# Kernel tuning notes

Hardware: AMD Instinct MI355X
Metric: run time of the kernel (lower is better)

The kernel has to match this reference:

```python
import jax, jax.numpy as jnp
import numpy as np

NUM_HEADS = 8
HEAD_DIM = 64
HIDDEN = 512
ROPE_THETA = 500000.0


def _make_rope(seq_len, head_dim, theta):
    inv_freq = 1.0 / (theta ** (np.arange(0, head_dim, 2, dtype=np.float32) / head_dim))
    t = np.arange(seq_len, dtype=np.float32)
    freqs = np.outer(t, inv_freq)                  # [S, hd/2]
    emb = np.concatenate([freqs, freqs], axis=-1)  # [S, hd]
    return jnp.asarray(np.cos(emb)), jnp.asarray(np.sin(emb))


def setup_inputs() -> dict:
    key = jax.random.key(0)
    ks = jax.random.split(key, 5)
    B, S, H = 1, 4096, HIDDEN
    num_registers = 32
    hidden_states = jax.random.normal(ks[0], (B, S, H), dtype=jnp.float32)
    scale = 0.02
    Wq = jax.random.normal(ks[1], (H, H), dtype=jnp.float32) * scale
    Wk = jax.random.normal(ks[2], (H, H), dtype=jnp.float32) * scale
    Wv = jax.random.normal(ks[3], (H, H), dtype=jnp.float32) * scale
    Wo = jax.random.normal(ks[4], (H, H), dtype=jnp.float32) * scale
    cos, sin = _make_rope(S - num_registers, HEAD_DIM, ROPE_THETA)
    return {"hidden_states": hidden_states, "Wq": Wq, "Wk": Wk, "Wv": Wv,
            "Wo": Wo, "cos": cos, "sin": sin, "num_registers": num_registers}


def _rotate_half(x):
    x1, x2 = jnp.split(x, 2, axis=-1)
    return jnp.concatenate([-x2, x1], axis=-1)


def _apply_rope(q, k, cos, sin):
    # cos/sin: [S_real, hd] broadcast over [B, H, S_real, hd]
    cos = cos[None, None]
    sin = sin[None, None]
    return q * cos + _rotate_half(q) * sin, k * cos + _rotate_half(k) * sin


def reference(hidden_states, Wq, Wk, Wv, Wo, cos, sin, num_registers):
    B, S, _ = hidden_states.shape
    def proj(W):
        # torch Linear: x @ W.T -> [B, S, H] -> [B, nh, S, hd]
        y = jnp.einsum('bsh,oh->bso', hidden_states, W)
        return y.reshape(B, S, NUM_HEADS, HEAD_DIM).transpose(0, 2, 1, 3)
    q, k, v = proj(Wq), proj(Wk), proj(Wv)

    if num_registers > 0:
        q_reg, q_real = q[:, :, :num_registers], q[:, :, num_registers:]
        k_reg, k_real = k[:, :, :num_registers], k[:, :, num_registers:]
        q_real, k_real = _apply_rope(q_real, k_real, cos, sin)
        q = jnp.concatenate([q_reg, q_real], axis=2)
        k = jnp.concatenate([k_reg, k_real], axis=2)
    else:
        q, k = _apply_rope(q, k, cos, sin)

    scale = 1.0 / jnp.sqrt(jnp.float32(HEAD_DIM))
    scores = jnp.einsum('bhqd,bhkd->bhqk', q, k) * scale  # [B, nh, S, S]
    causal = jnp.tril(jnp.ones((S, S), dtype=bool))
    scores = jnp.where(causal[None, None], scores, jnp.float32(-1e30))
    attn = jax.nn.softmax(scores, axis=-1)
    out = jnp.einsum('bhqk,bhkd->bhqd', attn, v)
    out = out.transpose(0, 2, 1, 3).reshape(B, S, HIDDEN)
    return jnp.einsum('bsh,oh->bso', out, Wo)
```

## Files before the change

kernel.cpp:

```cpp
#include <hip/hip_runtime.h>
#include <cstdint>
#include <cstddef>

#define S_LEN 4096
#define HID   512
#define NHEAD 8
#define HD    64
#define SCALE_LOG2E 0.1803368801111204f

typedef __bf16 bf16;
typedef __bf16 bf16x8 __attribute__((ext_vector_type(8)));
typedef __bf16 bf16x4 __attribute__((ext_vector_type(4)));
typedef float  f32x4  __attribute__((ext_vector_type(4)));

__global__ __launch_bounds__(256) void cvt_f32_bf16(const float* __restrict__ src,
                                                    bf16* __restrict__ dst, int n) {
    int i = (blockIdx.x * 256 + threadIdx.x) * 4;
    if (i + 3 < n) {
        const float4 v = *(const float4*)(src + i);
        bf16x4 o;
        o[0] = (bf16)v.x; o[1] = (bf16)v.y; o[2] = (bf16)v.z; o[3] = (bf16)v.w;
        *(bf16x4*)(dst + i) = o;
    }
}

__global__ __launch_bounds__(256) void cvt_w4(
    const float* __restrict__ s0, const float* __restrict__ s1,
    const float* __restrict__ s2, const float* __restrict__ s3,
    bf16* __restrict__ d0, bf16* __restrict__ d1,
    bf16* __restrict__ d2, bf16* __restrict__ d3) {
    const float* src; bf16* dst;
    switch (blockIdx.y) {
        case 0: src = s0; dst = d0; break;
        case 1: src = s1; dst = d1; break;
        case 2: src = s2; dst = d2; break;
        default: src = s3; dst = d3; break;
    }
    int i = (blockIdx.x * 256 + threadIdx.x) * 4;
    const float4 v = *(const float4*)(src + i);
    bf16x4 o;
    o[0] = (bf16)v.x; o[1] = (bf16)v.y; o[2] = (bf16)v.z; o[3] = (bf16)v.w;
    *(bf16x4*)(dst + i) = o;
}

#define BM 128
#define BN 128
#define BKK 64

__global__ __launch_bounds__(256) void gemm_qkv(
    const bf16* __restrict__ X,
    const bf16* __restrict__ W0, const bf16* __restrict__ W1, const bf16* __restrict__ W2,
    const float* __restrict__ cosT, const float* __restrict__ sinT,
    const int* __restrict__ nregp,
    bf16* __restrict__ Qh, bf16* __restrict__ Kh, bf16* __restrict__ Vt)
{
    const int z = blockIdx.z;
    const bf16* W = (z == 0) ? W0 : (z == 1 ? W1 : W2);
    const int m0 = blockIdx.y * BM, n0 = blockIdx.x * BN;
    __shared__ bf16 lA[BM][8][8];
    __shared__ bf16 lB[BN][8][8];
    const int tid = threadIdx.x;
    const int lane = tid & 63, w = tid >> 6;
    const int l16 = lane & 15, lc = lane >> 4, l7 = lane & 7;
    const int wm = (w & 1) * 64, wn = (w >> 1) * 64;
    f32x4 acc[4][4] = {};

    for (int k0 = 0; k0 < HID; k0 += BKK) {
        __syncthreads();
#pragma unroll
        for (int i = 0; i < 4; i++) {
            int uu = tid + 256 * i;
            int m = uu >> 3, c = uu & 7;
            *(float4*)(&lA[m][c ^ (m & 7)][0]) =
                *(const float4*)(X + (size_t)(m0 + m) * HID + k0 + 8 * c);
            *(float4*)(&lB[m][c ^ (m & 7)][0]) =
                *(const float4*)(W + (size_t)(n0 + m) * HID + k0 + 8 * c);
        }
        __syncthreads();
#pragma unroll
        for (int ks = 0; ks < 2; ks++) {
            bf16x8 af[4], bfr[4];
#pragma unroll
            for (int i = 0; i < 4; i++) {
                af[i]  = *(const bf16x8*)(&lA[wm + 16 * i + l16][(4 * ks + lc) ^ l7][0]);
                bfr[i] = *(const bf16x8*)(&lB[wn + 16 * i + l16][(4 * ks + lc) ^ l7][0]);
            }
#pragma unroll
            for (int i = 0; i < 4; i++)
#pragma unroll
                for (int j = 0; j < 4; j++)
                    acc[i][j] = __builtin_amdgcn_mfma_f32_16x16x32_bf16(
                        af[i], bfr[j], acc[i][j], 0, 0, 0);
        }
    }

    const int h = (n0 + wn) >> 6;
    if (z == 2) {
#pragma unroll
        for (int i = 0; i < 4; i++) {
            const int s0r = m0 + wm + 16 * i + 4 * lc;
#pragma unroll
            for (int j = 0; j < 4; j++) {
                const int dl = 16 * j + l16;
                bf16x4 o;
#pragma unroll
                for (int r = 0; r < 4; r++) o[r] = (bf16)acc[i][j][r];
                *(bf16x4*)(Vt + ((size_t)(h * HD + dl)) * S_LEN + s0r) = o;
            }
        }
    } else {
        const int nreg = *nregp;
        bf16* dst = (z == 0) ? Qh : Kh;
#pragma unroll
        for (int i = 0; i < 4; i++) {
            const int s0r = m0 + wm + 16 * i + 4 * lc;
#pragma unroll
            for (int r = 0; r < 4; r++) {
                const int s = s0r + r;
                float c0 = 1.f, sn0 = 0.f, c1 = 1.f, sn1 = 0.f;
                if (s >= nreg) {
                    const int p = s - nreg;
                    c0  = cosT[(size_t)p * HD + l16];
                    sn0 = sinT[(size_t)p * HD + l16];
                    c1  = cosT[(size_t)p * HD + 16 + l16];
                    sn1 = sinT[(size_t)p * HD + 16 + l16];
                }
                const float x0 = acc[i][0][r], x1 = acc[i][1][r];
                const float x2 = acc[i][2][r], x3 = acc[i][3][r];
                bf16* row = dst + ((size_t)h * S_LEN + s) * HD;
                row[l16]      = (bf16)(x0 * c0 - x2 * sn0);
                row[l16 + 16] = (bf16)(x1 * c1 - x3 * sn1);
                row[l16 + 32] = (bf16)(x2 * c0 + x0 * sn0);
                row[l16 + 48] = (bf16)(x3 * c1 + x1 * sn1);
            }
        }
    }
}

__global__ __launch_bounds__(256) void gemm_out(
    const bf16* __restrict__ X, const bf16* __restrict__ W,
    float* __restrict__ Y)
{
    const int m0 = blockIdx.y * BM, n0 = blockIdx.x * BN;
    __shared__ bf16 lA[BM][8][8];
    __shared__ bf16 lB[BN][8][8];
    const int tid = threadIdx.x;
    const int lane = tid & 63, w = tid >> 6;
    const int l16 = lane & 15, lc = lane >> 4, l7 = lane & 7;
    const int wm = (w & 1) * 64, wn = (w >> 1) * 64;
    f32x4 acc[4][4] = {};

    for (int k0 = 0; k0 < HID; k0 += BKK) {
        __syncthreads();
#pragma unroll
        for (int i = 0; i < 4; i++) {
            int uu = tid + 256 * i;
            int m = uu >> 3, c = uu & 7;
            *(float4*)(&lA[m][c ^ (m & 7)][0]) =
                *(const float4*)(X + (size_t)(m0 + m) * HID + k0 + 8 * c);
            *(float4*)(&lB[m][c ^ (m & 7)][0]) =
                *(const float4*)(W + (size_t)(n0 + m) * HID + k0 + 8 * c);
        }
        __syncthreads();
#pragma unroll
        for (int ks = 0; ks < 2; ks++) {
            bf16x8 af[4], bfr[4];
#pragma unroll
            for (int i = 0; i < 4; i++) {
                af[i]  = *(const bf16x8*)(&lA[wm + 16 * i + l16][(4 * ks + lc) ^ l7][0]);
                bfr[i] = *(const bf16x8*)(&lB[wn + 16 * i + l16][(4 * ks + lc) ^ l7][0]);
            }
#pragma unroll
            for (int i = 0; i < 4; i++)
#pragma unroll
                for (int j = 0; j < 4; j++)
                    acc[i][j] = __builtin_amdgcn_mfma_f32_16x16x32_bf16(
                        af[i], bfr[j], acc[i][j], 0, 0, 0);
        }
    }
#pragma unroll
    for (int i = 0; i < 4; i++) {
        int row = m0 + wm + 16 * i + 4 * lc;
#pragma unroll
        for (int j = 0; j < 4; j++) {
            int col = n0 + wn + 16 * j + l16;
#pragma unroll
            for (int r = 0; r < 4; r++)
                Y[(size_t)(row + r) * HID + col] = acc[i][j][r];
        }
    }
}

__global__ __launch_bounds__(256) void attn_part(
    const bf16* __restrict__ Qh, const bf16* __restrict__ Kh,
    const bf16* __restrict__ Vt, float* __restrict__ Opart,
    float* __restrict__ Lpart)
{
    const int h = blockIdx.x >> 1;
    const int ch = blockIdx.x & 1;
    const int bt = 63 - (int)blockIdx.y;
    const int qb = bt * 64;
    const int nkt = bt + 1;
    const int kmid = nkt >> 1;
    const int k0 = ch ? kmid : 0;
    const int k1 = ch ? nkt : kmid;
    const int tid = threadIdx.x;
    const int lane = tid & 63, w = tid >> 6;
    const int l16 = lane & 15, lc = lane >> 4, l7 = lane & 7;

    float* Op = Opart + ((size_t)(h * 64 + bt) * 2 + ch) * 4096;
    float* Lp = Lpart + ((size_t)(h * 64 + bt) * 2 + ch) * 64;

    if (k0 >= k1) {
        const f32x4 z = {0.f, 0.f, 0.f, 0.f};
#pragma unroll
        for (int i = 0; i < 4; i++)
            *(f32x4*)(Op + 4 * (tid + 256 * i)) = z;
        if (tid < 64) Lp[tid] = 0.f;
        return;
    }

    __shared__ bf16 lK[2][64][8][8];
    __shared__ bf16 lV[2][64][8][8];
    __shared__ bf16 lPT[4][16][76];

    const bf16* Kb_ = Kh + (size_t)h * S_LEN * HD;
    const bf16* Vb_ = Vt + (size_t)h * HD * S_LEN;

    int srow[2], scol[2];
#pragma unroll
    for (int i = 0; i < 2; i++) {
        int uu = tid + 256 * i;
        srow[i] = uu >> 3;
        scol[i] = uu & 7;
    }

    bf16x8 qf[2];
    {
        const bf16* qrow = Qh + (size_t)h * S_LEN * HD + (size_t)(qb + 16 * w + l16) * HD;
        qf[0] = *(const bf16x8*)(qrow + 8 * lc);
        qf[1] = *(const bf16x8*)(qrow + 32 + 8 * lc);
    }
    f32x4 oacc[4] = {};
    float l_sum = 0.f;

    {
        bf16x8 kr[2], vr[2];
#pragma unroll
        for (int i = 0; i < 2; i++) {
            kr[i] = *(const bf16x8*)(Kb_ + (size_t)(k0 * 64 + srow[i]) * HD + 8 * scol[i]);
            vr[i] = *(const bf16x8*)(Vb_ + (size_t)srow[i] * S_LEN + k0 * 64 + 8 * scol[i]);
        }
#pragma unroll
        for (int i = 0; i < 2; i++) {
            *(bf16x8*)(&lK[0][srow[i]][scol[i] ^ (srow[i] & 7)][0]) = kr[i];
            *(bf16x8*)(&lV[0][srow[i]][scol[i] ^ (srow[i] & 7)][0]) = vr[i];
        }
    }

    int cur = 0;
    for (int kt = k0; kt < k1; kt++) {
        __syncthreads();

        bf16x8 kr[2], vr[2];
        if (kt + 1 < k1) {
#pragma unroll
            for (int i = 0; i < 2; i++) {
                kr[i] = *(const bf16x8*)(Kb_ + (size_t)((kt + 1) * 64 + srow[i]) * HD +
                                         8 * scol[i]);
                vr[i] = *(const bf16x8*)(Vb_ + (size_t)srow[i] * S_LEN +
                                         (kt + 1) * 64 + 8 * scol[i]);
            }
        }

        f32x4 sacc[4] = {};
#pragma unroll
        for (int ks = 0; ks < 2; ks++)
#pragma unroll
            for (int j = 0; j < 4; j++) {
                bf16x8 kf = *(const bf16x8*)(&lK[cur][16 * j + l16][(4 * ks + lc) ^ l7][0]);
                sacc[j] = __builtin_amdgcn_mfma_f32_16x16x32_bf16(
                    kf, qf[ks], sacc[j], 0, 0, 0);
            }

        float pv[4][4];
#pragma unroll
        for (int j = 0; j < 4; j++)
#pragma unroll
            for (int r = 0; r < 4; r++)
                pv[j][r] = __builtin_amdgcn_exp2f(sacc[j][r] * SCALE_LOG2E);
        if (kt == nkt - 1) {
            const int qg = qb + 16 * w + l16;
#pragma unroll
            for (int j = 0; j < 4; j++)
#pragma unroll
                for (int r = 0; r < 4; r++) {
                    const int keyg = kt * 64 + 16 * j + 4 * lc + r;
                    if (keyg > qg) pv[j][r] = 0.f;
                }
        }
#pragma unroll
        for (int j = 0; j < 4; j++)
            l_sum += (pv[j][0] + pv[j][1]) + (pv[j][2] + pv[j][3]);

#pragma unroll
        for (int j = 0; j < 4; j++) {
            bf16x4 pp;
#pragma unroll
            for (int r = 0; r < 4; r++) pp[r] = (bf16)pv[j][r];
            *(bf16x4*)(&lPT[w][l16][16 * j + 4 * lc]) = pp;
        }
        bf16x8 pb[2];
#pragma unroll
        for (int ks = 0; ks < 2; ks++)
            pb[ks] = *(const bf16x8*)(&lPT[w][l16][32 * ks + 8 * lc]);

#pragma unroll
        for (int ks = 0; ks < 2; ks++)
#pragma unroll
            for (int j = 0; j < 4; j++) {
                bf16x8 vf = *(const bf16x8*)(&lV[cur][16 * j + l16][(4 * ks + lc) ^ l7][0]);
                oacc[j] = __builtin_amdgcn_mfma_f32_16x16x32_bf16(
                    vf, pb[ks], oacc[j], 0, 0, 0);
            }

        if (kt + 1 < k1) {
#pragma unroll
            for (int i = 0; i < 2; i++) {
                *(bf16x8*)(&lK[cur ^ 1][srow[i]][scol[i] ^ (srow[i] & 7)][0]) = kr[i];
                *(bf16x8*)(&lV[cur ^ 1][srow[i]][scol[i] ^ (srow[i] & 7)][0]) = vr[i];
            }
        }
        cur ^= 1;
    }

    l_sum += __shfl_xor(l_sum, 16, 64);
    l_sum += __shfl_xor(l_sum, 32, 64);
    if (lane < 16) Lp[16 * w + l16] = l_sum;

#pragma unroll
    for (int j = 0; j < 4; j++)
        *(f32x4*)(Op + (size_t)(16 * w + l16) * 64 + 16 * j + 4 * lc) = oacc[j];
}

__global__ __launch_bounds__(256) void attn_combine(
    const float* __restrict__ Opart, const float* __restrict__ Lpart,
    bf16* __restrict__ Ob)
{
    const int h = blockIdx.x, bt = blockIdx.y;
    const size_t base = (size_t)(h * 64 + bt) * 2;
    const float* O0 = Opart + base * 4096;
    const float* O1 = O0 + 4096;
    const float* L0 = Lpart + base * 64;
    const int t = threadIdx.x;
    const int q = t >> 2, dq = (t & 3) * 16;
    const float l = L0[q] + L0[64 + q];
    const float inv = 1.0f / l;
    bf16* out = Ob + (size_t)(bt * 64 + q) * HID + h * HD + dq;
#pragma unroll
    for (int g = 0; g < 2; g++) {
        bf16x8 o8;
#pragma unroll
        for (int e = 0; e < 2; e++) {
            f32x4 a = *(const f32x4*)(O0 + q * 64 + dq + 8 * g + 4 * e);
            f32x4 b = *(const f32x4*)(O1 + q * 64 + dq + 8 * g + 4 * e);
#pragma unroll
            for (int r = 0; r < 4; r++) o8[4 * e + r] = (bf16)((a[r] + b[r]) * inv);
        }
        *(bf16x8*)(out + 8 * g) = o8;
    }
}

extern "C" void kernel_launch(void* const* d_in, const int* in_sizes, int n_in,
                              void* d_out, int out_size, void* d_ws, size_t ws_size,
                              hipStream_t stream) {
    const float* hs   = (const float*)d_in[0];
    const float* Wq   = (const float*)d_in[1];
    const float* Wk   = (const float*)d_in[2];
    const float* Wv   = (const float*)d_in[3];
    const float* Wo   = (const float*)d_in[4];
    const float* cosT = (const float*)d_in[5];
    const float* sinT = (const float*)d_in[6];
    const int*   nreg = (const int*)d_in[7];

    char* ws = (char*)d_ws;
    const size_t MiB = 1 << 20;
    bf16*  Xb    = (bf16*)(ws);
    bf16*  Wqb   = (bf16*)(ws + 4 * MiB);
    bf16*  Wkb   = (bf16*)(ws + 4 * MiB + 512 * 1024);
    bf16*  Wvb   = (bf16*)(ws + 5 * MiB);
    bf16*  Wob   = (bf16*)(ws + 5 * MiB + 512 * 1024);
    bf16*  Qh    = (bf16*)(ws + 6 * MiB);
    bf16*  Kh    = (bf16*)(ws + 10 * MiB);
    bf16*  Vt    = (bf16*)(ws + 14 * MiB);
    bf16*  Ob    = (bf16*)(ws + 18 * MiB);
    float* Opart = (float*)(ws + 22 * MiB);
    float* Lpart = (float*)(ws + 38 * MiB);

    cvt_f32_bf16<<<2048, 256, 0, stream>>>(hs, Xb, S_LEN * HID);
    cvt_w4<<<dim3(256, 4), 256, 0, stream>>>(Wq, Wk, Wv, Wo, Wqb, Wkb, Wvb, Wob);

    gemm_qkv<<<dim3(4, 32, 3), 256, 0, stream>>>(Xb, Wqb, Wkb, Wvb,
                                                 cosT, sinT, nreg, Qh, Kh, Vt);
    attn_part<<<dim3(16, 64), 256, 0, stream>>>(Qh, Kh, Vt, Opart, Lpart);
    attn_combine<<<dim3(8, 64), 256, 0, stream>>>(Opart, Lpart, Ob);
    gemm_out<<<dim3(4, 32), 256, 0, stream>>>(Ob, Wob, (float*)d_out);
}
```

Before: 148.8 us.

## Fuse fp32-to-bf16 conversion into GEMM loads and shrink GEMM tiles

Removes the two standalone conversion kernels and has the QKV and output GEMMs read fp32 inputs and weights directly, converting to bf16 while staging into LDS. This drops two launches and the round trip of bf16 copies through memory. The QKV GEMM tile shrinks from 128x128 to 64x128 and the output GEMM tile to 64x64, so more blocks launch. In exchange each block reads twice as many fp32 bytes per element, and weights are re-read and re-converted by every block.

```diff
diff --git a/kernel.cpp b/kernel.cpp
--- a/kernel.cpp
+++ b/kernel.cpp
@@ -13,80 +13,61 @@
 typedef __bf16 bf16x4 __attribute__((ext_vector_type(4)));
 typedef float  f32x4  __attribute__((ext_vector_type(4)));
 
-__global__ __launch_bounds__(256) void cvt_f32_bf16(const float* __restrict__ src,
-                                                    bf16* __restrict__ dst, int n) {
-    int i = (blockIdx.x * 256 + threadIdx.x) * 4;
-    if (i + 3 < n) {
-        const float4 v = *(const float4*)(src + i);
-        bf16x4 o;
-        o[0] = (bf16)v.x; o[1] = (bf16)v.y; o[2] = (bf16)v.z; o[3] = (bf16)v.w;
-        *(bf16x4*)(dst + i) = o;
-    }
-}
-
-__global__ __launch_bounds__(256) void cvt_w4(
-    const float* __restrict__ s0, const float* __restrict__ s1,
-    const float* __restrict__ s2, const float* __restrict__ s3,
-    bf16* __restrict__ d0, bf16* __restrict__ d1,
-    bf16* __restrict__ d2, bf16* __restrict__ d3) {
-    const float* src; bf16* dst;
-    switch (blockIdx.y) {
-        case 0: src = s0; dst = d0; break;
-        case 1: src = s1; dst = d1; break;
-        case 2: src = s2; dst = d2; break;
-        default: src = s3; dst = d3; break;
-    }
-    int i = (blockIdx.x * 256 + threadIdx.x) * 4;
-    const float4 v = *(const float4*)(src + i);
-    bf16x4 o;
-    o[0] = (bf16)v.x; o[1] = (bf16)v.y; o[2] = (bf16)v.z; o[3] = (bf16)v.w;
-    *(bf16x4*)(dst + i) = o;
-}
-
-#define BM 128
-#define BN 128
-#define BKK 64
+__device__ __forceinline__ bf16x8 cvt8(float4 a, float4 b) {
+    bf16x8 o;
+    o[0] = (bf16)a.x; o[1] = (bf16)a.y; o[2] = (bf16)a.z; o[3] = (bf16)a.w;
+    o[4] = (bf16)b.x; o[5] = (bf16)b.y; o[6] = (bf16)b.z; o[7] = (bf16)b.w;
+    return o;
+}
 
 __global__ __launch_bounds__(256) void gemm_qkv(
-    const bf16* __restrict__ X,
-    const bf16* __restrict__ W0, const bf16* __restrict__ W1, const bf16* __restrict__ W2,
+    const float* __restrict__ Xf,
+    const float* __restrict__ W0, const float* __restrict__ W1, const float* __restrict__ W2,
     const float* __restrict__ cosT, const float* __restrict__ sinT,
     const int* __restrict__ nregp,
     bf16* __restrict__ Qh, bf16* __restrict__ Kh, bf16* __restrict__ Vt)
 {
     const int z = blockIdx.z;
-    const bf16* W = (z == 0) ? W0 : (z == 1 ? W1 : W2);
-    const int m0 = blockIdx.y * BM, n0 = blockIdx.x * BN;
-    __shared__ bf16 lA[BM][8][8];
-    __shared__ bf16 lB[BN][8][8];
+    const float* W = (z == 0) ? W0 : (z == 1 ? W1 : W2);
+    const int m0 = blockIdx.y * 64, n0 = blockIdx.x * 128;
+    __shared__ bf16 lA[64][8][8];
+    __shared__ bf16 lB[128][8][8];
     const int tid = threadIdx.x;
     const int lane = tid & 63, w = tid >> 6;
     const int l16 = lane & 15, lc = lane >> 4, l7 = lane & 7;
-    const int wm = (w & 1) * 64, wn = (w >> 1) * 64;
-    f32x4 acc[4][4] = {};
-
-    for (int k0 = 0; k0 < HID; k0 += BKK) {
-        __syncthreads();
+    const int wm = (w & 1) * 32, wn = (w >> 1) * 64;
+    f32x4 acc[2][4] = {};
+
+    for (int k0 = 0; k0 < HID; k0 += 64) {
+        __syncthreads();
+#pragma unroll
+        for (int i = 0; i < 2; i++) {
+            int uu = tid + 256 * i;
+            int m = uu >> 3, c = uu & 7;
+            const float* p = Xf + (size_t)(m0 + m) * HID + k0 + 8 * c;
+            *(bf16x8*)(&lA[m][c ^ (m & 7)][0]) =
+                cvt8(*(const float4*)p, *(const float4*)(p + 4));
+        }
 #pragma unroll
         for (int i = 0; i < 4; i++) {
             int uu = tid + 256 * i;
             int m = uu >> 3, c = uu & 7;
-            *(float4*)(&lA[m][c ^ (m & 7)][0]) =
-                *(const float4*)(X + (size_t)(m0 + m) * HID + k0 + 8 * c);
-            *(float4*)(&lB[m][c ^ (m & 7)][0]) =
-                *(const float4*)(W + (size_t)(n0 + m) * HID + k0 + 8 * c);
+            const float* p = W + (size_t)(n0 + m) * HID + k0 + 8 * c;
+            *(bf16x8*)(&lB[m][c ^ (m & 7)][0]) =
+                cvt8(*(const float4*)p, *(const float4*)(p + 4));
         }
         __syncthreads();
 #pragma unroll
         for (int ks = 0; ks < 2; ks++) {
-            bf16x8 af[4], bfr[4];
-#pragma unroll
-            for (int i = 0; i < 4; i++) {
+            bf16x8 af[2], bfr[4];
+#pragma unroll
+            for (int i = 0; i < 2; i++)
                 af[i]  = *(const bf16x8*)(&lA[wm + 16 * i + l16][(4 * ks + lc) ^ l7][0]);
-                bfr[i] = *(const bf16x8*)(&lB[wn + 16 * i + l16][(4 * ks + lc) ^ l7][0]);
-            }
-#pragma unroll
-            for (int i = 0; i < 4; i++)
+#pragma unroll
+            for (int j = 0; j < 4; j++)
+                bfr[j] = *(const bf16x8*)(&lB[wn + 16 * j + l16][(4 * ks + lc) ^ l7][0]);
+#pragma unroll
+            for (int i = 0; i < 2; i++)
 #pragma unroll
                 for (int j = 0; j < 4; j++)
                     acc[i][j] = __builtin_amdgcn_mfma_f32_16x16x32_bf16(
@@ -97,7 +78,7 @@
     const int h = (n0 + wn) >> 6;
     if (z == 2) {
 #pragma unroll
-        for (int i = 0; i < 4; i++) {
+        for (int i = 0; i < 2; i++) {
             const int s0r = m0 + wm + 16 * i + 4 * lc;
 #pragma unroll
             for (int j = 0; j < 4; j++) {
@@ -112,7 +93,7 @@
         const int nreg = *nregp;
         bf16* dst = (z == 0) ? Qh : Kh;
 #pragma unroll
-        for (int i = 0; i < 4; i++) {
+        for (int i = 0; i < 2; i++) {
             const int s0r = m0 + wm + 16 * i + 4 * lc;
 #pragma unroll
             for (int r = 0; r < 4; r++) {
@@ -138,51 +119,57 @@
 }
 
 __global__ __launch_bounds__(256) void gemm_out(
-    const bf16* __restrict__ X, const bf16* __restrict__ W,
+    const bf16* __restrict__ X, const float* __restrict__ Wf,
     float* __restrict__ Y)
 {
-    const int m0 = blockIdx.y * BM, n0 = blockIdx.x * BN;
-    __shared__ bf16 lA[BM][8][8];
-    __shared__ bf16 lB[BN][8][8];
+    const int m0 = blockIdx.y * 64, n0 = blockIdx.x * 64;
+    __shared__ bf16 lA[64][8][8];
+    __shared__ bf16 lB[64][8][8];
     const int tid = threadIdx.x;
     const int lane = tid & 63, w = tid >> 6;
     const int l16 = lane & 15, lc = lane >> 4, l7 = lane & 7;
-    const int wm = (w & 1) * 64, wn = (w >> 1) * 64;
-    f32x4 acc[4][4] = {};
-
-    for (int k0 = 0; k0 < HID; k0 += BKK) {
-        __syncthreads();
-#pragma unroll
-        for (int i = 0; i < 4; i++) {
+    const int wm = (w & 1) * 32, wn = (w >> 1) * 32;
+    f32x4 acc[2][2] = {};
+
+    for (int k0 = 0; k0 < HID; k0 += 64) {
+        __syncthreads();
+#pragma unroll
+        for (int i = 0; i < 2; i++) {
             int uu = tid + 256 * i;
             int m = uu >> 3, c = uu & 7;
-            *(float4*)(&lA[m][c ^ (m & 7)][0]) =
-                *(const float4*)(X + (size_t)(m0 + m) * HID + k0 + 8 * c);
-            *(float4*)(&lB[m][c ^ (m & 7)][0]) =
-                *(const float4*)(W + (size_t)(n0 + m) * HID + k0 + 8 * c);
+            *(bf16x8*)(&lA[m][c ^ (m & 7)][0]) =
+                *(const bf16x8*)(X + (size_t)(m0 + m) * HID + k0 + 8 * c);
+        }
+#pragma unroll
+        for (int i = 0; i < 2; i++) {
+            int uu = tid + 256 * i;
+            int m = uu >> 3, c = uu & 7;
+            const float* p = Wf + (size_t)(n0 + m) * HID + k0 + 8 * c;
+            *(bf16x8*)(&lB[m][c ^ (m & 7)][0]) =
+                cvt8(*(const float4*)p, *(const float4*)(p + 4));
         }
         __syncthreads();
 #pragma unroll
         for (int ks = 0; ks < 2; ks++) {
-            bf16x8 af[4], bfr[4];
-#pragma unroll
-            for (int i = 0; i < 4; i++) {
+            bf16x8 af[2], bfr[2];
+#pragma unroll
+            for (int i = 0; i < 2; i++) {
                 af[i]  = *(const bf16x8*)(&lA[wm + 16 * i + l16][(4 * ks + lc) ^ l7][0]);
                 bfr[i] = *(const bf16x8*)(&lB[wn + 16 * i + l16][(4 * ks + lc) ^ l7][0]);
             }
 #pragma unroll
-            for (int i = 0; i < 4; i++)
-#pragma unroll
-                for (int j = 0; j < 4; j++)
+            for (int i = 0; i < 2; i++)
+#pragma unroll
+                for (int j = 0; j < 2; j++)
                     acc[i][j] = __builtin_amdgcn_mfma_f32_16x16x32_bf16(
                         af[i], bfr[j], acc[i][j], 0, 0, 0);
         }
     }
 #pragma unroll
-    for (int i = 0; i < 4; i++) {
+    for (int i = 0; i < 2; i++) {
         int row = m0 + wm + 16 * i + 4 * lc;
 #pragma unroll
-        for (int j = 0; j < 4; j++) {
+        for (int j = 0; j < 2; j++) {
             int col = n0 + wn + 16 * j + l16;
 #pragma unroll
             for (int r = 0; r < 4; r++)
@@ -385,24 +372,16 @@
 
     char* ws = (char*)d_ws;
     const size_t MiB = 1 << 20;
-    bf16*  Xb    = (bf16*)(ws);
-    bf16*  Wqb   = (bf16*)(ws + 4 * MiB);
-    bf16*  Wkb   = (bf16*)(ws + 4 * MiB + 512 * 1024);
-    bf16*  Wvb   = (bf16*)(ws + 5 * MiB);
-    bf16*  Wob   = (bf16*)(ws + 5 * MiB + 512 * 1024);
-    bf16*  Qh    = (bf16*)(ws + 6 * MiB);
-    bf16*  Kh    = (bf16*)(ws + 10 * MiB);
-    bf16*  Vt    = (bf16*)(ws + 14 * MiB);
-    bf16*  Ob    = (bf16*)(ws + 18 * MiB);
-    float* Opart = (float*)(ws + 22 * MiB);
-    float* Lpart = (float*)(ws + 38 * MiB);
-
-    cvt_f32_bf16<<<2048, 256, 0, stream>>>(hs, Xb, S_LEN * HID);
-    cvt_w4<<<dim3(256, 4), 256, 0, stream>>>(Wq, Wk, Wv, Wo, Wqb, Wkb, Wvb, Wob);
-
-    gemm_qkv<<<dim3(4, 32, 3), 256, 0, stream>>>(Xb, Wqb, Wkb, Wvb,
+    bf16*  Qh    = (bf16*)(ws);
+    bf16*  Kh    = (bf16*)(ws + 4 * MiB);
+    bf16*  Vt    = (bf16*)(ws + 8 * MiB);
+    bf16*  Ob    = (bf16*)(ws + 12 * MiB);
+    float* Opart = (float*)(ws + 16 * MiB);
+    float* Lpart = (float*)(ws + 32 * MiB);
+
+    gemm_qkv<<<dim3(4, 64, 3), 256, 0, stream>>>(hs, Wq, Wk, Wv,
                                                  cosT, sinT, nreg, Qh, Kh, Vt);
     attn_part<<<dim3(16, 64), 256, 0, stream>>>(Qh, Kh, Vt, Opart, Lpart);
     attn_combine<<<dim3(8, 64), 256, 0, stream>>>(Opart, Lpart, Ob);
-    gemm_out<<<dim3(4, 32), 256, 0, stream>>>(Ob, Wob, (float*)d_out);
-}
+    gemm_out<<<dim3(8, 64), 256, 0, stream>>>(Ob, Wo, (float*)d_out);
+}
```

After: 148.8 us. About the same (-0.0%).
